# Optimization experiments

Hardware: AMD Instinct MI355X
Metric: run time of the kernel (lower is better)

The kernel has to match this reference:

```python
import jax, jax.numpy as jnp
import numpy as np

B, N, F_IN, F_OUT = 8, 2048, 128, 128
ALPHA = 0.1  # leaky-relu negative slope
NEG = -9e15


def setup_inputs() -> dict:
    key = jax.random.key(0)
    k1, k2, k3, k4, k5, k6 = jax.random.split(key, 6)
    s = 1.0 / np.sqrt(F_OUT)
    return {
        "x1": jax.random.normal(k1, (B, N, F_IN), dtype=jnp.float32),
        "x2": jax.random.normal(k2, (B, N, F_IN), dtype=jnp.float32),
        "cross_weight": jax.random.uniform(k3, (F_IN, F_OUT), minval=-s, maxval=s, dtype=jnp.float32),
        "friend_weight": jax.random.uniform(k4, (F_IN, F_OUT), minval=-s, maxval=s, dtype=jnp.float32),
        "self_weight": jax.random.uniform(k5, (F_IN, F_OUT), minval=-s, maxval=s, dtype=jnp.float32),
        "att_weight": jax.random.uniform(k6, (2 * F_OUT, 1), minval=-1.0, maxval=1.0, dtype=jnp.float32),
    }


def _one_set(xq, x_others, cross_weight, friend_weight, self_weight, att_weight):
    # GAT-style additive attention for one set against cross-set + friend supports.
    fo = cross_weight.shape[1]
    a_q, a_k = att_weight[:fo], att_weight[fo:]  # split additive-attention vector
    cross = jnp.concatenate([xo @ cross_weight for xo in x_others], axis=1)  # [B, M, F]
    friend = xq @ friend_weight                                              # [B, Nq, F]
    h = jnp.concatenate([cross, friend], axis=1)                             # [B, Nk, F]
    s_q = (friend @ a_q)[..., 0]  # [B, Nq]
    s_k = (h @ a_k)[..., 0]       # [B, Nk]
    e = jax.nn.leaky_relu(s_q[:, :, None] + s_k[:, None, :], negative_slope=ALPHA)  # [B, Nq, Nk]
    nq, m = xq.shape[1], cross.shape[1]
    # mask: all cross-set keys allowed; friend keys masked on the diagonal (no self-edge)
    mask = jnp.concatenate([jnp.ones((nq, m), dtype=e.dtype),
                            1.0 - jnp.eye(nq, dtype=e.dtype)], axis=1)
    att = jax.nn.softmax(jnp.where(mask > 0, e, NEG), axis=-1)  # [B, Nq, Nk]
    out = jnp.einsum('bqk,bkf->bqf', att, h)                    # [B, Nq, F]
    return out + xq @ self_weight


def reference(x1, x2, cross_weight, friend_weight, self_weight, att_weight):
    out1 = _one_set(x1, [x2], cross_weight, friend_weight, self_weight, att_weight)
    out2 = _one_set(x2, [x1], cross_weight, friend_weight, self_weight, att_weight)
    return (out1, out2)
```

## Files before the change

### kernel.cpp

```cpp
#include <hip/hip_runtime.h>
#include <hip/hip_bf16.h>
#include <stdint.h>

typedef __attribute__((ext_vector_type(8))) short short8;
typedef __attribute__((ext_vector_type(16))) float f32x16;

#define NB 8
#define NN 2048
#define NF 128
#define NK 4096

#define LRA 0.1f
#define L2E 1.4426950408889634f

#define OFF_HT   0u
#define OFF_WCT  16777216u
#define OFF_WFT  16809984u
#define OFF_WST  16842752u
#define OFF_U1   16875520u
#define OFF_U2   16876032u
#define OFF_U3   16876544u
#define OFF_SQ   16877056u
#define OFF_SK   17008128u

__device__ __forceinline__ short f2bf(float f){
  __bf16 h = (__bf16)f;
  return __builtin_bit_cast(short, h);
}
__device__ __forceinline__ short8 pack8(float4 a, float4 b){
  short8 r;
  r[0]=f2bf(a.x); r[1]=f2bf(a.y); r[2]=f2bf(a.z); r[3]=f2bf(a.w);
  r[4]=f2bf(b.x); r[5]=f2bf(b.y); r[6]=f2bf(b.z); r[7]=f2bf(b.w);
  return r;
}

typedef const __attribute__((address_space(1))) unsigned int* gas_t;
typedef __attribute__((address_space(3))) unsigned int* las_t;
__device__ __forceinline__ void gload_lds16(const void* g, void* l){
  __builtin_amdgcn_global_load_lds((gas_t)g, (las_t)l, 16, 0, 0);
}

__global__ __launch_bounds__(256) void k_prep(const float* __restrict__ Wc,
                                              const float* __restrict__ Wf,
                                              const float* __restrict__ Ws,
                                              const float* __restrict__ att,
                                              char* __restrict__ ws){
  short* WcT = (short*)(ws + OFF_WCT);
  short* WfT = (short*)(ws + OFF_WFT);
  short* WsT = (short*)(ws + OFF_WST);
  float* u1  = (float*)(ws + OFF_U1);
  float* u2  = (float*)(ws + OFF_U2);
  float* u3  = (float*)(ws + OFF_U3);
  int t = threadIdx.x;
  for (int e = t; e < NF*NF; e += 256){
    int col = e >> 7, k = e & 127;
    WcT[col*NF + k] = f2bf(Wc[k*NF + col]);
    WfT[col*NF + k] = f2bf(Wf[k*NF + col]);
    WsT[col*NF + k] = f2bf(Ws[k*NF + col]);
  }
  if (t < NF){
    float s1=0.f, s2=0.f, s3=0.f;
    for (int c = 0; c < NF; c++){
      float aq = att[c], ak = att[NF + c];
      float wf = Wf[t*NF + c], wc = Wc[t*NF + c];
      s1 += wf*aq; s2 += wc*ak; s3 += wf*ak;
    }
    u1[t]=s1; u2[t]=s2; u3[t]=s3;
  }
}

__global__ __launch_bounds__(256) void k_build(const float* __restrict__ x1,
                                               const float* __restrict__ x2,
                                               char* __restrict__ ws){
  int bid = blockIdx.x;
  int xid  = bid >> 7;
  int b    = (bid >> 4) & 7;
  int tile = bid & 15;
  int tid = threadIdx.x, wid = tid >> 6, lane = tid & 63;
  int l31 = lane & 31, khalf = lane >> 5;
  int r0 = tile*128 + wid*32;
  int row = r0 + l31;

  const float* x = xid ? x2 : x1;
  const float* u1 = (const float*)(ws + OFF_U1);
  const float* u2 = (const float*)(ws + OFF_U2);
  const float* u3 = (const float*)(ws + OFF_U3);
  const float* xrow = x + (size_t)(b*NN + row)*NF;

  short8 aF[8];
  float p1=0.f, p2=0.f, p3=0.f;
  #pragma unroll
  for (int ks = 0; ks < 8; ks++){
    int k0 = ks*16 + khalf*8;
    float4 xa = *(const float4*)(xrow + k0);
    float4 xb = *(const float4*)(xrow + k0 + 4);
    float4 a1 = *(const float4*)(u1 + k0), b1 = *(const float4*)(u1 + k0 + 4);
    float4 a2 = *(const float4*)(u2 + k0), b2 = *(const float4*)(u2 + k0 + 4);
    float4 a3 = *(const float4*)(u3 + k0), b3 = *(const float4*)(u3 + k0 + 4);
    p1 += xa.x*a1.x + xa.y*a1.y + xa.z*a1.z + xa.w*a1.w
        + xb.x*b1.x + xb.y*b1.y + xb.z*b1.z + xb.w*b1.w;
    p2 += xa.x*a2.x + xa.y*a2.y + xa.z*a2.z + xa.w*a2.w
        + xb.x*b2.x + xb.y*b2.y + xb.z*b2.z + xb.w*b2.w;
    p3 += xa.x*a3.x + xa.y*a3.y + xa.z*a3.z + xa.w*a3.w
        + xb.x*b3.x + xb.y*b3.y + xb.z*b3.z + xb.w*b3.w;
    aF[ks] = pack8(xa, xb);
  }
  p1 += __shfl_xor(p1, 32);
  p2 += __shfl_xor(p2, 32);
  p3 += __shfl_xor(p3, 32);
  if (lane < 32){
    float* sq = (float*)(ws + OFF_SQ);
    float* sk = (float*)(ws + OFF_SK);
    sq[(xid*NB + b)*NN + row] = p1;
    sk[(xid*NB + b)*NK + NN + row] = p3;
    sk[((1 - xid)*NB + b)*NK + row] = p2;
  }

  short* hT = (short*)(ws + OFF_HT);
  #pragma unroll
  for (int g = 0; g < 2; g++){
    const short* W = g ? (const short*)(ws + OFF_WFT) : (const short*)(ws + OFF_WCT);
    int dset = g ? xid : (1 - xid);
    int kb2  = (g ? NN : 0) + r0;
    f32x16 acc[4] = {};
    #pragma unroll
    for (int ks = 0; ks < 8; ks++){
      #pragma unroll
      for (int cb = 0; cb < 4; cb++){
        short8 bF = *(const short8*)(W + (cb*32 + l31)*NF + ks*16 + khalf*8);
        acc[cb] = __builtin_amdgcn_mfma_f32_32x32x16_bf16(aF[ks], bF, acc[cb], 0, 0, 0);
      }
    }
    short* hbase = hT + (size_t)(dset*NB + b)*NF*NK;
    #pragma unroll
    for (int cb = 0; cb < 4; cb++){
      short* hc = hbase + (size_t)(cb*32 + l31)*NK;
      #pragma unroll
      for (int g4 = 0; g4 < 4; g4++){
        int kr = kb2 + g4*8 + khalf*4;
        uint2 v;
        v.x = (unsigned)(unsigned short)f2bf(acc[cb][4*g4+0]) |
              ((unsigned)(unsigned short)f2bf(acc[cb][4*g4+1]) << 16);
        v.y = (unsigned)(unsigned short)f2bf(acc[cb][4*g4+2]) |
              ((unsigned)(unsigned short)f2bf(acc[cb][4*g4+3]) << 16);
        *(uint2*)(hc + kr) = v;
      }
    }
  }
}

__global__ __launch_bounds__(256) void k_attn(const float* __restrict__ x1,
                                              const float* __restrict__ x2,
                                              const char* __restrict__ ws,
                                              float* __restrict__ out){
  __shared__ float skb[NK];
  __shared__ __align__(16) char stg[2][16384];
  __shared__ float wmax[4];

  int hw = blockIdx.x;
  int bid = (hw & 7)*32 + (hw >> 3);
  int set = bid >> 7, b = (bid >> 4) & 7, qt = bid & 15;
  int tid = threadIdx.x, wid = tid >> 6, lane = tid & 63;
  int l31 = lane & 31, khalf = lane >> 5;

  const short* hT  = (const short*)(ws + OFF_HT) + (size_t)(set*NB + b)*NF*NK;
  const float* skg = (const float*)(ws + OFF_SK) + (set*NB + b)*NK;
  const float* sqg = (const float*)(ws + OFF_SQ) + (set*NB + b)*NN;
  const short* WsT = (const short*)(ws + OFF_WST);

  float mx = -3.0e38f;
  #pragma unroll
  for (int i = 0; i < 4; i++){
    int idx = i*1024 + tid*4;
    float4 v = *(const float4*)(skg + idx);
    *(float4*)(skb + idx) = v;
    mx = fmaxf(mx, fmaxf(fmaxf(v.x, v.y), fmaxf(v.z, v.w)));
  }
  #pragma unroll
  for (int d = 1; d < 64; d <<= 1) mx = fmaxf(mx, __shfl_xor(mx, d));
  if (lane == 0) wmax[wid] = mx;

  auto stage = [&](int ch, int bi){
    #pragma unroll
    for (int i = 0; i < 4; i++){
      int q = (wid*4 + i)*64 + lane;
      int col = q >> 3, k16 = q & 7;
      int srcc = k16 ^ (col & 7);
      gload_lds16((const void*)(hT + col*NK + ch*64 + srcc*8),
                  (void*)&stg[bi][(wid*4 + i)*1024]);
    }
  };
  stage(0, 0);
  __syncthreads();

  float skmax = fmaxf(fmaxf(wmax[0], wmax[1]), fmaxf(wmax[2], wmax[3]));
  int q0w = qt*128 + wid*32;
  int row = q0w + l31;
  float sqv = sqg[row];
  float t0 = sqv + skmax;
  float m = fmaxf(t0, LRA*t0);
  float moff = m * L2E;
  int kdiag = NN + row;
  int chd = (NN + q0w) >> 6;
  int ksd = (q0w & 63) >> 4;

  f32x16 acc[4] = {};
  float zacc = 0.f;

  for (int ch = 0; ch < 64; ch++){
    int bi = ch & 1;
    if (ch < 63) stage(ch + 1, bi ^ 1);
    #pragma unroll
    for (int ks = 0; ks < 4; ks++){
      const float* skp = skb + ch*64 + ks*16 + khalf*8;
      float4 sa = *(const float4*)skp;
      float4 sb = *(const float4*)(skp + 4);
      float sv[8] = {sa.x, sa.y, sa.z, sa.w, sb.x, sb.y, sb.z, sb.w};
      float wv[8];
      #pragma unroll
      for (int j = 0; j < 8; j++){
        float t = sqv + sv[j];
        float lr = fmaxf(t, LRA*t);
        wv[j] = __builtin_amdgcn_exp2f(__builtin_fmaf(lr, L2E, -moff));
      }
      if (ch == chd && (ks & ~1) == ksd){
        int kg0 = ch*64 + ks*16 + khalf*8;
        #pragma unroll
        for (int j = 0; j < 8; j++) wv[j] = (kg0 + j == kdiag) ? 0.f : wv[j];
      }
      #pragma unroll
      for (int j = 0; j < 8; j++) zacc += wv[j];
      short8 aw;
      #pragma unroll
      for (int j = 0; j < 8; j++) aw[j] = f2bf(wv[j]);
      #pragma unroll
      for (int cb = 0; cb < 4; cb++){
        int col = cb*32 + l31;
        int slot = (ks*2 + khalf) ^ (col & 7);
        short8 bF = *(const short8*)&stg[bi][col*128 + slot*16];
        acc[cb] = __builtin_amdgcn_mfma_f32_32x32x16_bf16(aw, bF, acc[cb], 0, 0, 0);
      }
    }
    __syncthreads();
  }

  zacc += __shfl_xor(zacc, 32);
  float rz = 1.0f / zacc;
  float rzv[16];
  #pragma unroll
  for (int r = 0; r < 16; r++){
    int rowc = (r & 3) + 8*(r >> 2) + 4*khalf;
    rzv[r] = __shfl(rz, rowc);
  }
  #pragma unroll
  for (int cb = 0; cb < 4; cb++)
    #pragma unroll
    for (int r = 0; r < 16; r++) acc[cb][r] *= rzv[r];

  const float* x = set ? x2 : x1;
  const float* xrow = x + (size_t)(b*NN + row)*NF;
  #pragma unroll
  for (int ks = 0; ks < 8; ks++){
    int k0 = ks*16 + khalf*8;
    float4 xa = *(const float4*)(xrow + k0);
    float4 xb = *(const float4*)(xrow + k0 + 4);
    short8 aF = pack8(xa, xb);
    #pragma unroll
    for (int cb = 0; cb < 4; cb++){
      short8 bF = *(const short8*)(WsT + (cb*32 + l31)*NF + k0);
      acc[cb] = __builtin_amdgcn_mfma_f32_32x32x16_bf16(aF, bF, acc[cb], 0, 0, 0);
    }
  }

  float* op = out + (size_t)(set*NB + b)*NN*NF;
  #pragma unroll
  for (int cb = 0; cb < 4; cb++){
    #pragma unroll
    for (int r = 0; r < 16; r++){
      int rowc = (r & 3) + 8*(r >> 2) + 4*khalf;
      op[(size_t)(q0w + rowc)*NF + cb*32 + l31] = acc[cb][r];
    }
  }
}

extern "C" void kernel_launch(void* const* d_in, const int* in_sizes, int n_in,
                              void* d_out, int out_size, void* d_ws, size_t ws_size,
                              hipStream_t stream){
  const float* x1  = (const float*)d_in[0];
  const float* x2  = (const float*)d_in[1];
  const float* Wc  = (const float*)d_in[2];
  const float* Wf  = (const float*)d_in[3];
  const float* Ws  = (const float*)d_in[4];
  const float* att = (const float*)d_in[5];
  char* ws = (char*)d_ws;
  float* out = (float*)d_out;

  k_prep<<<dim3(1),   dim3(256), 0, stream>>>(Wc, Wf, Ws, att, ws);
  k_build<<<dim3(256), dim3(256), 0, stream>>>(x1, x2, ws);
  k_attn<<<dim3(256), dim3(256), 0, stream>>>(x1, x2, ws, out);
}
```

Baseline: 211.1 us.

## Split attention keys across two wave groups, triple-buffer staging, parallelize prep

The attention kernel now runs 512 threads per block. Two groups of four waves each cover half of the key range, and their partial accumulators and row sums are combined through LDS at the end. Staging becomes a 3-deep buffer per group, managed with explicit vmcnt waits and raw barriers. Scores are pre-scaled by log2(e) in the build kernel so the inner leaky-relu plus exp needs fewer operations. The prep kernel is spread over 13 blocks with an LDS-tiled transpose and wave-reduced dot products instead of a single serial block. This adds LDS pressure, around 100KB per block, and more hand-written synchronization to get right.

New measurement: 179.7 us. -14.9%, faster.

```diff
diff --git a/kernel.cpp b/kernel.cpp
--- a/kernel.cpp
+++ b/kernel.cpp
@@ -9,8 +9,6 @@
 #define NN 2048
 #define NF 128
 #define NK 4096
-
-#define LRA 0.1f
 #define L2E 1.4426950408889634f
 
 #define OFF_HT   0u
@@ -45,27 +43,45 @@
                                               const float* __restrict__ Ws,
                                               const float* __restrict__ att,
                                               char* __restrict__ ws){
-  short* WcT = (short*)(ws + OFF_WCT);
-  short* WfT = (short*)(ws + OFF_WFT);
-  short* WsT = (short*)(ws + OFF_WST);
-  float* u1  = (float*)(ws + OFF_U1);
-  float* u2  = (float*)(ws + OFF_U2);
-  float* u3  = (float*)(ws + OFF_U3);
-  int t = threadIdx.x;
-  for (int e = t; e < NF*NF; e += 256){
-    int col = e >> 7, k = e & 127;
-    WcT[col*NF + k] = f2bf(Wc[k*NF + col]);
-    WfT[col*NF + k] = f2bf(Wf[k*NF + col]);
-    WsT[col*NF + k] = f2bf(Ws[k*NF + col]);
-  }
-  if (t < NF){
-    float s1=0.f, s2=0.f, s3=0.f;
-    for (int c = 0; c < NF; c++){
-      float aq = att[c], ak = att[NF + c];
-      float wf = Wf[t*NF + c], wc = Wc[t*NF + c];
-      s1 += wf*aq; s2 += wc*ak; s3 += wf*ak;
-    }
-    u1[t]=s1; u2[t]=s2; u3[t]=s3;
+  int bidx = blockIdx.x, tid = threadIdx.x;
+  if (bidx < 12){
+    __shared__ float tile[32][129];
+    int m = bidx >> 2, tno = bidx & 3;
+    const float* W = (m == 0) ? Wc : ((m == 1) ? Wf : Ws);
+    short* WT = (short*)(ws + ((m == 0) ? OFF_WCT : ((m == 1) ? OFF_WFT : OFF_WST)));
+    int r0 = tno*32;
+    #pragma unroll
+    for (int i = 0; i < 16; i++){
+      int e = tid + i*256;
+      tile[e >> 7][e & 127] = W[(r0 + (e >> 7))*NF + (e & 127)];
+    }
+    __syncthreads();
+    #pragma unroll
+    for (int i = 0; i < 16; i++){
+      int o = tid + i*256;
+      int col = o >> 5, rr = o & 31;
+      WT[col*NF + r0 + rr] = f2bf(tile[rr][col]);
+    }
+  } else {
+    int wid = tid >> 6, lane = tid & 63;
+    float aq0 = att[lane],      aq1 = att[64 + lane];
+    float ak0 = att[NF + lane], ak1 = att[NF + 64 + lane];
+    float* u1 = (float*)(ws + OFF_U1);
+    float* u2 = (float*)(ws + OFF_U2);
+    float* u3 = (float*)(ws + OFF_U3);
+    for (int j = 0; j < 32; j++){
+      int r = wid*32 + j;
+      float wf0 = Wf[r*NF + lane], wf1 = Wf[r*NF + 64 + lane];
+      float wc0 = Wc[r*NF + lane], wc1 = Wc[r*NF + 64 + lane];
+      float s1 = wf0*aq0 + wf1*aq1;
+      float s2 = wc0*ak0 + wc1*ak1;
+      float s3 = wf0*ak0 + wf1*ak1;
+      #pragma unroll
+      for (int d = 1; d < 64; d <<= 1){
+        s1 += __shfl_xor(s1, d); s2 += __shfl_xor(s2, d); s3 += __shfl_xor(s3, d);
+      }
+      if (lane == 0){ u1[r] = s1; u2[r] = s2; u3[r] = s3; }
+    }
   }
 }
 
@@ -111,9 +127,9 @@
   if (lane < 32){
     float* sq = (float*)(ws + OFF_SQ);
     float* sk = (float*)(ws + OFF_SK);
-    sq[(xid*NB + b)*NN + row] = p1;
-    sk[(xid*NB + b)*NK + NN + row] = p3;
-    sk[((1 - xid)*NB + b)*NK + row] = p2;
+    sq[(xid*NB + b)*NN + row] = p1*L2E;
+    sk[(xid*NB + b)*NK + NN + row] = p3*L2E;
+    sk[((1 - xid)*NB + b)*NK + row] = p2*L2E;
   }
 
   short* hT = (short*)(ws + OFF_HT);
@@ -149,18 +165,19 @@
   }
 }
 
-__global__ __launch_bounds__(256) void k_attn(const float* __restrict__ x1,
+__global__ __launch_bounds__(512) void k_attn(const float* __restrict__ x1,
                                               const float* __restrict__ x2,
                                               const char* __restrict__ ws,
                                               float* __restrict__ out){
   __shared__ float skb[NK];
-  __shared__ __align__(16) char stg[2][16384];
-  __shared__ float wmax[4];
+  __shared__ __align__(16) char stg[6*16384];
+  __shared__ float wmax[8];
 
   int hw = blockIdx.x;
   int bid = (hw & 7)*32 + (hw >> 3);
   int set = bid >> 7, b = (bid >> 4) & 7, qt = bid & 15;
   int tid = threadIdx.x, wid = tid >> 6, lane = tid & 63;
+  int grp = wid >> 2, rw = wid & 3;
   int l31 = lane & 31, khalf = lane >> 5;
 
   const short* hT  = (const short*)(ws + OFF_HT) + (size_t)(set*NB + b)*NF*NK;
@@ -168,10 +185,25 @@
   const float* sqg = (const float*)(ws + OFF_SQ) + (set*NB + b)*NN;
   const short* WsT = (const short*)(ws + OFF_WST);
 
+  auto stage = [&](int li, int bufi){
+    char* dst = stg + (grp*3 + bufi)*16384;
+    int ch = grp*32 + li;
+    #pragma unroll
+    for (int i = 0; i < 4; i++){
+      int q = (rw*4 + i)*64 + lane;
+      int col = q >> 3, k16 = q & 7;
+      int srcc = k16 ^ (col & 7);
+      gload_lds16((const void*)(hT + col*NK + ch*64 + srcc*8),
+                  (void*)(dst + (rw*4 + i)*1024));
+    }
+  };
+
+  stage(0, 0);
+  stage(1, 1);
   float mx = -3.0e38f;
   #pragma unroll
-  for (int i = 0; i < 4; i++){
-    int idx = i*1024 + tid*4;
+  for (int i = 0; i < 2; i++){
+    int idx = i*2048 + tid*4;
     float4 v = *(const float4*)(skg + idx);
     *(float4*)(skb + idx) = v;
     mx = fmaxf(mx, fmaxf(fmaxf(v.x, v.y), fmaxf(v.z, v.w)));
@@ -179,27 +211,20 @@
   #pragma unroll
   for (int d = 1; d < 64; d <<= 1) mx = fmaxf(mx, __shfl_xor(mx, d));
   if (lane == 0) wmax[wid] = mx;
-
-  auto stage = [&](int ch, int bi){
-    #pragma unroll
-    for (int i = 0; i < 4; i++){
-      int q = (wid*4 + i)*64 + lane;
-      int col = q >> 3, k16 = q & 7;
-      int srcc = k16 ^ (col & 7);
-      gload_lds16((const void*)(hT + col*NK + ch*64 + srcc*8),
-                  (void*)&stg[bi][(wid*4 + i)*1024]);
-    }
-  };
-  stage(0, 0);
-  __syncthreads();
-
-  float skmax = fmaxf(fmaxf(wmax[0], wmax[1]), fmaxf(wmax[2], wmax[3]));
-  int q0w = qt*128 + wid*32;
+  asm volatile("s_waitcnt lgkmcnt(0)" ::: "memory");
+  asm volatile("s_barrier" ::: "memory");
+
+  float skmax = wmax[0];
+  #pragma unroll
+  for (int i = 1; i < 8; i++) skmax = fmaxf(skmax, wmax[i]);
+
+  int q0w = qt*128 + rw*32;
   int row = q0w + l31;
   float sqv = sqg[row];
   float t0 = sqv + skmax;
-  float m = fmaxf(t0, LRA*t0);
-  float moff = m * L2E;
+  float moff = fmaxf(t0, 0.1f*t0);
+  float sqm = sqv - moff;
+  float c9  = -0.9f*moff;
   int kdiag = NN + row;
   int chd = (NN + q0w) >> 6;
   int ksd = (q0w & 63) >> 4;
@@ -207,21 +232,29 @@
   f32x16 acc[4] = {};
   float zacc = 0.f;
 
-  for (int ch = 0; ch < 64; ch++){
-    int bi = ch & 1;
-    if (ch < 63) stage(ch + 1, bi ^ 1);
+  int bs = 2, bc = 0;
+  for (int it = 0; it < 32; ++it){
+    if (it < 30){
+      stage(it + 2, bs);
+      asm volatile("s_waitcnt vmcnt(8)" ::: "memory");
+    } else if (it == 30){
+      asm volatile("s_waitcnt vmcnt(4)" ::: "memory");
+    } else {
+      asm volatile("s_waitcnt vmcnt(0)" ::: "memory");
+    }
+    asm volatile("s_barrier" ::: "memory");
+
+    int ch = grp*32 + it;
+    const char* buf = stg + (grp*3 + bc)*16384;
     #pragma unroll
     for (int ks = 0; ks < 4; ks++){
       const float* skp = skb + ch*64 + ks*16 + khalf*8;
-      float4 sa = *(const float4*)skp;
-      float4 sb = *(const float4*)(skp + 4);
-      float sv[8] = {sa.x, sa.y, sa.z, sa.w, sb.x, sb.y, sb.z, sb.w};
       float wv[8];
       #pragma unroll
       for (int j = 0; j < 8; j++){
-        float t = sqv + sv[j];
-        float lr = fmaxf(t, LRA*t);
-        wv[j] = __builtin_amdgcn_exp2f(__builtin_fmaf(lr, L2E, -moff));
+        float p = skp[j] + sqm;
+        float qn = __builtin_fmaf(0.1f, p, c9);
+        wv[j] = __builtin_amdgcn_exp2f(fmaxf(p, qn));
       }
       if (ch == chd && (ks & ~1) == ksd){
         int kg0 = ch*64 + ks*16 + khalf*8;
@@ -237,48 +270,68 @@
       for (int cb = 0; cb < 4; cb++){
         int col = cb*32 + l31;
         int slot = (ks*2 + khalf) ^ (col & 7);
-        short8 bF = *(const short8*)&stg[bi][col*128 + slot*16];
+        short8 bF = *(const short8*)(buf + col*128 + slot*16);
         acc[cb] = __builtin_amdgcn_mfma_f32_32x32x16_bf16(aw, bF, acc[cb], 0, 0, 0);
       }
     }
-    __syncthreads();
-  }
-
-  zacc += __shfl_xor(zacc, 32);
-  float rz = 1.0f / zacc;
-  float rzv[16];
-  #pragma unroll
-  for (int r = 0; r < 16; r++){
-    int rowc = (r & 3) + 8*(r >> 2) + 4*khalf;
-    rzv[r] = __shfl(rz, rowc);
-  }
-  #pragma unroll
-  for (int cb = 0; cb < 4; cb++)
-    #pragma unroll
-    for (int r = 0; r < 16; r++) acc[cb][r] *= rzv[r];
-
-  const float* x = set ? x2 : x1;
-  const float* xrow = x + (size_t)(b*NN + row)*NF;
-  #pragma unroll
-  for (int ks = 0; ks < 8; ks++){
-    int k0 = ks*16 + khalf*8;
-    float4 xa = *(const float4*)(xrow + k0);
-    float4 xb = *(const float4*)(xrow + k0 + 4);
-    short8 aF = pack8(xa, xb);
-    #pragma unroll
-    for (int cb = 0; cb < 4; cb++){
-      short8 bF = *(const short8*)(WsT + (cb*32 + l31)*NF + k0);
-      acc[cb] = __builtin_amdgcn_mfma_f32_32x32x16_bf16(aF, bF, acc[cb], 0, 0, 0);
-    }
-  }
-
-  float* op = out + (size_t)(set*NB + b)*NN*NF;
-  #pragma unroll
-  for (int cb = 0; cb < 4; cb++){
+    asm volatile("s_barrier" ::: "memory");
+    bs = (bs == 2) ? 0 : bs + 1;
+    bc = (bc == 2) ? 0 : bc + 1;
+  }
+
+  float* xch = (float*)stg;
+  float* zx  = skb;
+  if (grp == 1){
+    #pragma unroll
+    for (int cb = 0; cb < 4; cb++)
+      #pragma unroll
+      for (int r = 0; r < 16; r++)
+        xch[(cb*16 + r)*256 + rw*64 + lane] = acc[cb][r];
+    zx[rw*64 + lane] = zacc;
+  }
+  __syncthreads();
+  if (grp == 0){
+    #pragma unroll
+    for (int cb = 0; cb < 4; cb++)
+      #pragma unroll
+      for (int r = 0; r < 16; r++)
+        acc[cb][r] += xch[(cb*16 + r)*256 + rw*64 + lane];
+    zacc += zx[rw*64 + lane];
+    zacc += __shfl_xor(zacc, 32);
+    float rz = 1.0f / zacc;
+    float rzv[16];
     #pragma unroll
     for (int r = 0; r < 16; r++){
       int rowc = (r & 3) + 8*(r >> 2) + 4*khalf;
-      op[(size_t)(q0w + rowc)*NF + cb*32 + l31] = acc[cb][r];
+      rzv[r] = __shfl(rz, rowc);
+    }
+    #pragma unroll
+    for (int cb = 0; cb < 4; cb++)
+      #pragma unroll
+      for (int r = 0; r < 16; r++) acc[cb][r] *= rzv[r];
+
+    const float* x = set ? x2 : x1;
+    const float* xrow = x + (size_t)(b*NN + row)*NF;
+    #pragma unroll
+    for (int ks8 = 0; ks8 < 8; ks8++){
+      int k0 = ks8*16 + khalf*8;
+      float4 xa = *(const float4*)(xrow + k0);
+      float4 xb = *(const float4*)(xrow + k0 + 4);
+      short8 aF = pack8(xa, xb);
+      #pragma unroll
+      for (int cb = 0; cb < 4; cb++){
+        short8 bF = *(const short8*)(WsT + (cb*32 + l31)*NF + k0);
+        acc[cb] = __builtin_amdgcn_mfma_f32_32x32x16_bf16(aF, bF, acc[cb], 0, 0, 0);
+      }
+    }
+    float* op = out + (size_t)(set*NB + b)*NN*NF;
+    #pragma unroll
+    for (int cb = 0; cb < 4; cb++){
+      #pragma unroll
+      for (int r = 0; r < 16; r++){
+        int rowc = (r & 3) + 8*(r >> 2) + 4*khalf;
+        op[(size_t)(q0w + rowc)*NF + cb*32 + l31] = acc[cb][r];
+      }
     }
   }
 }
@@ -295,7 +348,7 @@
   char* ws = (char*)d_ws;
   float* out = (float*)d_out;
 
-  k_prep<<<dim3(1),   dim3(256), 0, stream>>>(Wc, Wf, Ws, att, ws);
+  k_prep<<<dim3(13),  dim3(256), 0, stream>>>(Wc, Wf, Ws, att, ws);
   k_build<<<dim3(256), dim3(256), 0, stream>>>(x1, x2, ws);
-  k_attn<<<dim3(256), dim3(256), 0, stream>>>(x1, x2, ws, out);
-}
+  k_attn<<<dim3(256), dim3(512), 0, stream>>>(x1, x2, ws, out);
+}
```
